# Kernel optimization log

Hardware: AMD Instinct MI355X
Metric: run time of the kernel (lower is better)

## Reference

```python
import jax, jax.numpy as jnp
import numpy as np

N_FEATS = 9       # OGB atom feature columns
VOCAB = 119       # per-feature embedding vocab (max OGB atom vocab)
HIDDEN = 128
NUM_HEADS = 8
HEAD_DIM = HIDDEN // NUM_HEADS


def setup_inputs() -> dict:
    key = jax.random.key(0)
    ks = jax.random.split(key, 12)
    N, K = 50000, 16
    X = jax.random.randint(ks[0], (N, N_FEATS), 0, VOCAB)
    nbr_idx = jax.random.randint(ks[1], (N, K), 0, N)
    nbr_mask = jax.random.randint(ks[2], (N, K), 0, 2).astype(bool)
    atom_emb = jax.random.normal(ks[3], (N_FEATS, VOCAB, HIDDEN), jnp.float32) * 0.02
    s = 1.0 / np.sqrt(HIDDEN)
    Wq = jax.random.normal(ks[4], (HIDDEN, HIDDEN), jnp.float32) * s
    bq = jnp.zeros((HIDDEN,), jnp.float32)
    Wk = jax.random.normal(ks[5], (HIDDEN, HIDDEN), jnp.float32) * s
    bk = jnp.zeros((HIDDEN,), jnp.float32)
    Wv = jax.random.normal(ks[6], (HIDDEN, HIDDEN), jnp.float32) * s
    bv = jnp.zeros((HIDDEN,), jnp.float32)
    return {"X": X, "nbr_idx": nbr_idx, "nbr_mask": nbr_mask,
            "atom_emb": atom_emb, "Wq": Wq, "bq": bq,
            "Wk": Wk, "bk": bk, "Wv": Wv, "bv": bv}


def reference(X, nbr_idx, nbr_mask, atom_emb, Wq, bq, Wk, bk, Wv, bv):
    N = X.shape[0]
    # AtomEncoder: sum per-feature embedding lookups -> [N, HIDDEN]
    h = jnp.sum(atom_emb[jnp.arange(N_FEATS)[None, :], X], axis=1)
    scaling = HEAD_DIM ** -0.5
    q = (h @ Wq + bq).reshape(N, NUM_HEADS, HEAD_DIM) * scaling
    k = (h @ Wk + bk).reshape(N, NUM_HEADS, HEAD_DIM)
    v = (h @ Wv + bv).reshape(N, NUM_HEADS, HEAD_DIM)
    # ELL-format sparse attention: gather padded neighbor k/v -> [N, K, H, D]
    k_n = k[nbr_idx]
    v_n = v[nbr_idx]
    scores = jnp.einsum('nhd,nkhd->nkh', q, k_n)          # [N, K, H]
    scores = jnp.where(nbr_mask[..., None], scores, -1e9)
    attn = jax.nn.softmax(scores, axis=1)                 # softmax over neighbors
    out = jnp.einsum('nkh,nkhd->nhd', attn, v_n)          # [N, H, D]
    return out.reshape(N, HIDDEN)
```

## Files before the change

kernel.cpp:

```cpp
#include <hip/hip_runtime.h>
#include <hip/hip_bf16.h>

#define NFEAT 9
#define VOCAB 119
#define HIDDEN 128
#define NHEAD 8
#define HDIM 16
#define KNBR 16

typedef __attribute__((ext_vector_type(8))) short short8;
typedef __attribute__((ext_vector_type(4))) float f32x4;

__device__ __forceinline__ void load_lds16(const void* g, void* l) {
    __builtin_amdgcn_global_load_lds((const __attribute__((address_space(1))) void*)g,
                                     (__attribute__((address_space(3))) void*)l, 16, 0, 0);
}

template <int OFFS>
__device__ __forceinline__ float swz_xor(float v) {
    int r = __builtin_amdgcn_ds_swizzle(__float_as_int(v), OFFS);
    return __int_as_float(r);
}

__global__ void fill_kernel(float* out, int n, float val) {
    int i = blockIdx.x * blockDim.x + threadIdx.x;
    if (i < n) out[i] = val;
}

__global__ __launch_bounds__(256) void wt_kernel(
    const float* __restrict__ Wq, const float* __restrict__ Wk,
    const float* __restrict__ Wv, short* __restrict__ Wt)
{
    int mat = blockIdx.x >> 2, tile = blockIdx.x & 3;
    const float* W = (mat == 0) ? Wq : (mat == 1) ? Wk : Wv;
    __shared__ float ls[32 * HIDDEN];
    int tid = threadIdx.x;
    int cc0 = tile * 32;
    #pragma unroll
    for (int j = 0; j < 16; ++j) {
        int idx = j * 256 + tid;
        ls[idx] = W[(size_t)cc0 * HIDDEN + idx];
    }
    __syncthreads();
    int c = tid & 127, hf = tid >> 7;
    unsigned int ob[8];
    #pragma unroll
    for (int j = 0; j < 8; ++j) {
        int ccl = hf * 16 + 2 * j;
        __hip_bfloat16 b0 = __float2bfloat16(ls[ccl * HIDDEN + c]);
        __hip_bfloat16 b1 = __float2bfloat16(ls[(ccl + 1) * HIDDEN + c]);
        ob[j] = (unsigned int)*reinterpret_cast<unsigned short*>(&b0)
              | ((unsigned int)*reinterpret_cast<unsigned short*>(&b1) << 16);
    }
    unsigned int* dst = reinterpret_cast<unsigned int*>(
        Wt + (size_t)mat * HIDDEN * HIDDEN + (size_t)c * HIDDEN + cc0 + hf * 16);
    #pragma unroll
    for (int j = 0; j < 8; ++j) dst[j] = ob[j];
}

#define MT 32
#define HBS 136

__global__ __launch_bounds__(256, 3) void qkv_kernel(
    const int* __restrict__ X, const float* __restrict__ emb,
    const short* __restrict__ Wt,
    const float* __restrict__ bq, const float* __restrict__ bk,
    const float* __restrict__ bv,
    float* __restrict__ qf, __hip_bfloat16* __restrict__ kv, int N)
{
    __shared__ __align__(16) short hb[MT * HBS];
    __shared__ int xs[MT * NFEAT];

    const int tid = threadIdx.x;
    const int n0 = blockIdx.x * MT;

    for (int i = tid; i < MT * NFEAT; i += 256) {
        int n = n0 + i / NFEAT;
        int v = (n < N) ? X[(size_t)n * NFEAT + (i % NFEAT)] : 0;
        xs[i] = min(max(v, 0), VOCAB - 1);
    }
    __syncthreads();

    {
        const int cg = tid & 31;
        const int slot = tid >> 5;
        #pragma unroll
        for (int i = 0; i < 4; ++i) {
            int nl = slot * 4 + i;
            float4 acc = {0.f, 0.f, 0.f, 0.f};
            #pragma unroll
            for (int f = 0; f < NFEAT; ++f) {
                const float4 e = *reinterpret_cast<const float4*>(
                    &emb[((size_t)f * VOCAB + xs[nl * NFEAT + f]) * HIDDEN + cg * 4]);
                acc.x += e.x; acc.y += e.y; acc.z += e.z; acc.w += e.w;
            }
            __hip_bfloat162 p0 = __float22bfloat162_rn(make_float2(acc.x, acc.y));
            __hip_bfloat162 p1 = __float22bfloat162_rn(make_float2(acc.z, acc.w));
            uint2 u;
            u.x = *reinterpret_cast<unsigned int*>(&p0);
            u.y = *reinterpret_cast<unsigned int*>(&p1);
            *reinterpret_cast<uint2*>(&hb[nl * HBS + cg * 4]) = u;
        }
    }
    __syncthreads();

    const int wave = tid >> 6, lane = tid & 63;
    const int l15 = lane & 15, quad = lane >> 4;

    short8 b[2][3][4];
    float bias[2][3];
    #pragma unroll
    for (int g = 0; g < 2; ++g) {
        const int n = (wave * 2 + g) * 16 + l15;
        #pragma unroll
        for (int mat = 0; mat < 3; ++mat) {
            #pragma unroll
            for (int k0 = 0; k0 < 4; ++k0)
                b[g][mat][k0] = *reinterpret_cast<const short8*>(
                    &Wt[(size_t)mat * HIDDEN * HIDDEN + n * HIDDEN + k0 * 32 + quad * 8]);
            bias[g][mat] = (mat == 0) ? bq[n] : (mat == 1) ? bk[n] : bv[n];
        }
    }

    #pragma unroll
    for (int mt = 0; mt < 2; ++mt) {
        const int mloc = mt * 16 + l15;
        short8 a[4];
        #pragma unroll
        for (int k0 = 0; k0 < 4; ++k0)
            a[k0] = *reinterpret_cast<const short8*>(
                &hb[mloc * HBS + k0 * 32 + quad * 8]);
        #pragma unroll
        for (int g = 0; g < 2; ++g) {
            const int n = (wave * 2 + g) * 16 + l15;
            f32x4 acc[3] = {{0.f,0.f,0.f,0.f},{0.f,0.f,0.f,0.f},{0.f,0.f,0.f,0.f}};
            #pragma unroll
            for (int mat = 0; mat < 3; ++mat)
                #pragma unroll
                for (int k0 = 0; k0 < 4; ++k0)
                    acc[mat] = __builtin_amdgcn_mfma_f32_16x16x32_bf16(
                        a[k0], b[g][mat][k0], acc[mat], 0, 0, 0);
            #pragma unroll
            for (int mat = 0; mat < 3; ++mat) {
                #pragma unroll
                for (int r = 0; r < 4; ++r) {
                    int node = n0 + mt * 16 + quad * 4 + r;
                    if (node < N) {
                        float val = acc[mat][r] + bias[g][mat];
                        if (mat == 0)      qf[(size_t)node * HIDDEN + n] = val * 0.25f;
                        else if (mat == 1) kv[(size_t)node * 256 + n] = __float2bfloat16(val);
                        else               kv[(size_t)node * 256 + 128 + n] = __float2bfloat16(val);
                    }
                }
            }
        }
    }
}

#define NPB2 2
#define PAIRW 520

__global__ __launch_bounds__(256) void attn_kernel(
    const int* __restrict__ nbr_idx, const int* __restrict__ nbr_mask,
    const float* __restrict__ qf, const __hip_bfloat16* __restrict__ kv,
    float* __restrict__ out, int N)
{
    __shared__ __align__(16) __hip_bfloat16 kvp[NPB2][8][PAIRW];
    __shared__ float sl[NPB2][KNBR][NHEAD + 1];
    __shared__ int idxl[NPB2][KNBR];
    __shared__ int mskl[NPB2][KNBR];

    const int tid = threadIdx.x;
    const int local = tid >> 7;
    const int t = tid & 127;
    int n = blockIdx.x * NPB2 + local;
    if (n >= N) n = N - 1;

    if (t < KNBR) {
        int iv = nbr_idx[(size_t)n * KNBR + t];
        idxl[local][t] = min(max(iv, 0), N - 1);
        mskl[local][t] = nbr_mask[(size_t)n * KNBR + t];
    }
    __syncthreads();

    const int hh = t >> 4;
    const int kk = t & 15;

    float qr[HDIM];
    {
        const float4* qp = reinterpret_cast<const float4*>(
            qf + (size_t)n * HIDDEN + hh * HDIM);
        #pragma unroll
        for (int c4 = 0; c4 < 4; ++c4) {
            float4 qv = qp[c4];
            qr[4 * c4 + 0] = qv.x; qr[4 * c4 + 1] = qv.y;
            qr[4 * c4 + 2] = qv.z; qr[4 * c4 + 3] = qv.w;
        }
    }

    {
        const int w2 = t >> 6;
        const int l = t & 63;
        #pragma unroll
        for (int j = 0; j < 4; ++j) {
            int pair = 2 * j + w2;
            int r = pair * 2 + (l >> 5);
            bool khalf = (l & 31) < 16;
            if (!khalf || mskl[local][r]) {
                const short* src = (const short*)kv
                    + (size_t)idxl[local][r] * 256 + (size_t)(l & 31) * 8;
                load_lds16(src, &kvp[local][pair][0]);
            }
        }
    }
    __syncthreads();

    {
        const short8* kb = reinterpret_cast<const short8*>(
            &kvp[local][kk >> 1][(kk & 1) * 256 + hh * HDIM]);
        short8 k0 = kb[0], k1 = kb[1];
        const __hip_bfloat162* kp0 = reinterpret_cast<const __hip_bfloat162*>(&k0);
        const __hip_bfloat162* kp1 = reinterpret_cast<const __hip_bfloat162*>(&k1);
        float s = 0.f;
        #pragma unroll
        for (int d2 = 0; d2 < 4; ++d2) {
            float2 f0 = __bfloat1622float2(kp0[d2]);
            float2 f1 = __bfloat1622float2(kp1[d2]);
            s += qr[2 * d2] * f0.x + qr[2 * d2 + 1] * f0.y;
            s += qr[8 + 2 * d2] * f1.x + qr[8 + 2 * d2 + 1] * f1.y;
        }
        if (!mskl[local][kk]) s = -1e9f;
        float m = s;
        m = fmaxf(m, swz_xor<0x041F>(m));
        m = fmaxf(m, swz_xor<0x081F>(m));
        m = fmaxf(m, swz_xor<0x101F>(m));
        m = fmaxf(m, swz_xor<0x201F>(m));
        float e = __expf(s - m);
        float d = e;
        d += swz_xor<0x041F>(d);
        d += swz_xor<0x081F>(d);
        d += swz_xor<0x101F>(d);
        d += swz_xor<0x201F>(d);
        sl[local][kk][hh] = e / d;
    }
    __syncthreads();

    {
        const int dd = kk;
        float o = 0.f;
        #pragma unroll
        for (int j = 0; j < KNBR; ++j) {
            float w = sl[local][j][hh];
            float vv = __bfloat162float(
                kvp[local][j >> 1][(j & 1) * 256 + HIDDEN + hh * HDIM + dd]);
            o += w * vv;
        }
        out[(size_t)n * HIDDEN + t] = o;
    }
}

extern "C" void kernel_launch(void* const* d_in, const int* in_sizes, int n_in,
                              void* d_out, int out_size, void* d_ws, size_t ws_size,
                              hipStream_t stream)
{
    float* out = (float*)d_out;

    bool ok = (n_in == 10);
    int N = ok ? in_sizes[0] / NFEAT : 0;
    ok = ok && N > 0 && in_sizes[0] == N * NFEAT
            && in_sizes[1] == N * KNBR
            && in_sizes[2] == N * KNBR
            && in_sizes[3] == NFEAT * VOCAB * HIDDEN
            && in_sizes[4] == HIDDEN * HIDDEN && in_sizes[5] == HIDDEN
            && in_sizes[6] == HIDDEN * HIDDEN && in_sizes[7] == HIDDEN
            && in_sizes[8] == HIDDEN * HIDDEN && in_sizes[9] == HIDDEN
            && out_size == N * HIDDEN;
    if (!ok) {
        fill_kernel<<<(out_size + 255) / 256, 256, 0, stream>>>(out, out_size, 0.0f);
        return;
    }
    size_t need = (size_t)N * 1024 + 3 * HIDDEN * HIDDEN * sizeof(short);
    if (ws_size < need) {
        fill_kernel<<<(out_size + 255) / 256, 256, 0, stream>>>(out, out_size, 1.0f);
        return;
    }

    const int* X        = (const int*)d_in[0];
    const int* nbr_idx  = (const int*)d_in[1];
    const int* nbr_mask = (const int*)d_in[2];
    const float* emb = (const float*)d_in[3];
    const float* Wq  = (const float*)d_in[4];
    const float* bq  = (const float*)d_in[5];
    const float* Wk  = (const float*)d_in[6];
    const float* bk  = (const float*)d_in[7];
    const float* Wv  = (const float*)d_in[8];
    const float* bv  = (const float*)d_in[9];

    float* qf = (float*)d_ws;
    __hip_bfloat16* kv =
        (__hip_bfloat16*)((char*)d_ws + (size_t)N * HIDDEN * sizeof(float));
    short* Wt = (short*)((char*)d_ws + (size_t)N * 1024);

    wt_kernel<<<12, 256, 0, stream>>>(Wq, Wk, Wv, Wt);
    qkv_kernel<<<(N + MT - 1) / MT, 256, 0, stream>>>(
        X, emb, Wt, bq, bk, bv, qf, kv, N);
    attn_kernel<<<(N + NPB2 - 1) / NPB2, 256, 0, stream>>>(
        nbr_idx, nbr_mask, qf, kv, out, N);
}
```

Before: 168.3 us.

## Stage only K rows in LDS and load V straight to registers

The attention kernel now stages only the masked neighbor K rows into LDS via global_load_lds. V values are loaded directly from global memory into registers per thread, 16 neighbors each, and issued before the q load so they overlap with the K staging and score phase. Softmax weights are stored head-major so the output phase reads them as float4. This cuts LDS footprint and traffic but loads V for masked neighbors too, using scalar 2-byte global loads that may coalesce less well than the prior 16-byte LDS DMA.

```diff
diff --git a/kernel.cpp b/kernel.cpp
--- a/kernel.cpp
+++ b/kernel.cpp
@@ -158,16 +158,16 @@
 }
 
 #define NPB2 2
-#define PAIRW 520
+#define KGW 520
 
 __global__ __launch_bounds__(256) void attn_kernel(
     const int* __restrict__ nbr_idx, const int* __restrict__ nbr_mask,
     const float* __restrict__ qf, const __hip_bfloat16* __restrict__ kv,
     float* __restrict__ out, int N)
 {
-    __shared__ __align__(16) __hip_bfloat16 kvp[NPB2][8][PAIRW];
-    __shared__ float sl[NPB2][KNBR][NHEAD + 1];
-    __shared__ int idxl[NPB2][KNBR];
+    __shared__ __align__(16) __hip_bfloat16 kl[NPB2][4][KGW];
+    __shared__ __align__(16) float sl[NPB2][NHEAD][20];
+    __shared__ __align__(16) int idxl[NPB2][KNBR];
     __shared__ int mskl[NPB2][KNBR];
 
     const int tid = threadIdx.x;
@@ -186,6 +186,40 @@
     const int hh = t >> 4;
     const int kk = t & 15;
 
+    int idxr[KNBR];
+    {
+        const int4* ip = reinterpret_cast<const int4*>(&idxl[local][0]);
+        #pragma unroll
+        for (int m4 = 0; m4 < 4; ++m4) {
+            int4 iv = ip[m4];
+            idxr[4 * m4 + 0] = iv.x; idxr[4 * m4 + 1] = iv.y;
+            idxr[4 * m4 + 2] = iv.z; idxr[4 * m4 + 3] = iv.w;
+        }
+    }
+    const int mymsk = mskl[local][kk];
+
+    {
+        const int w2 = t >> 6;
+        const int l = t & 63;
+        #pragma unroll
+        for (int j2 = 0; j2 < 2; ++j2) {
+            int g = j2 * 2 + w2;
+            int r = g * 4 + (l >> 4);
+            if (mskl[local][r]) {
+                const short* src = (const short*)kv
+                    + (size_t)idxl[local][r] * 256 + (size_t)(l & 15) * 8;
+                load_lds16(src, &kl[local][g][0]);
+            }
+        }
+    }
+
+    float vr[KNBR];
+    #pragma unroll
+    for (int j = 0; j < KNBR; ++j) {
+        unsigned int u = *((const unsigned short*)kv + (size_t)idxr[j] * 256 + 128 + t);
+        vr[j] = __uint_as_float(u << 16);
+    }
+
     float qr[HDIM];
     {
         const float4* qp = reinterpret_cast<const float4*>(
@@ -197,27 +231,12 @@
             qr[4 * c4 + 2] = qv.z; qr[4 * c4 + 3] = qv.w;
         }
     }
-
-    {
-        const int w2 = t >> 6;
-        const int l = t & 63;
-        #pragma unroll
-        for (int j = 0; j < 4; ++j) {
-            int pair = 2 * j + w2;
-            int r = pair * 2 + (l >> 5);
-            bool khalf = (l & 31) < 16;
-            if (!khalf || mskl[local][r]) {
-                const short* src = (const short*)kv
-                    + (size_t)idxl[local][r] * 256 + (size_t)(l & 31) * 8;
-                load_lds16(src, &kvp[local][pair][0]);
-            }
-        }
-    }
-    __syncthreads();
-
-    {
+    __syncthreads();
+
+    {
+        const int g = kk >> 2, rg = kk & 3;
         const short8* kb = reinterpret_cast<const short8*>(
-            &kvp[local][kk >> 1][(kk & 1) * 256 + hh * HDIM]);
+            &kl[local][g][rg * 128 + hh * HDIM]);
         short8 k0 = kb[0], k1 = kb[1];
         const __hip_bfloat162* kp0 = reinterpret_cast<const __hip_bfloat162*>(&k0);
         const __hip_bfloat162* kp1 = reinterpret_cast<const __hip_bfloat162*>(&k1);
@@ -229,7 +248,7 @@
             s += qr[2 * d2] * f0.x + qr[2 * d2 + 1] * f0.y;
             s += qr[8 + 2 * d2] * f1.x + qr[8 + 2 * d2 + 1] * f1.y;
         }
-        if (!mskl[local][kk]) s = -1e9f;
+        if (!mymsk) s = -1e9f;
         float m = s;
         m = fmaxf(m, swz_xor<0x041F>(m));
         m = fmaxf(m, swz_xor<0x081F>(m));
@@ -241,19 +260,18 @@
         d += swz_xor<0x081F>(d);
         d += swz_xor<0x101F>(d);
         d += swz_xor<0x201F>(d);
-        sl[local][kk][hh] = e / d;
-    }
-    __syncthreads();
-
-    {
-        const int dd = kk;
+        sl[local][hh][kk] = e / d;
+    }
+    __syncthreads();
+
+    {
         float o = 0.f;
-        #pragma unroll
-        for (int j = 0; j < KNBR; ++j) {
-            float w = sl[local][j][hh];
-            float vv = __bfloat162float(
-                kvp[local][j >> 1][(j & 1) * 256 + HIDDEN + hh * HDIM + dd]);
-            o += w * vv;
+        const float4* wp = reinterpret_cast<const float4*>(&sl[local][hh][0]);
+        #pragma unroll
+        for (int m4 = 0; m4 < 4; ++m4) {
+            float4 w4 = wp[m4];
+            o += w4.x * vr[4 * m4 + 0] + w4.y * vr[4 * m4 + 1]
+               + w4.z * vr[4 * m4 + 2] + w4.w * vr[4 * m4 + 3];
         }
         out[(size_t)n * HIDDEN + t] = o;
     }
```

Result: no change. 166.1 us (-1.3%).
